# Optimization experiments

Hardware: AMD Instinct MI355X
Metric: run time of the kernel (lower is better)

## Reference

```python
import jax, jax.numpy as jnp
import numpy as np

EMBED = 1024
HEADS = 16
HEAD_DIM = EMBED // HEADS
FF = 4096
EPS = 1e-5


def layer_norm(x, g, b):
    mu = jnp.mean(x, axis=-1, keepdims=True)
    var = jnp.mean(jnp.square(x - mu), axis=-1, keepdims=True)
    return (x - mu) * jax.lax.rsqrt(var + EPS) * g + b


def setup_inputs() -> dict:
    key = jax.random.key(0)
    ks = jax.random.split(key, 16)
    s = 0.02
    x = jax.random.normal(ks[0], (4, 2048, EMBED), dtype=jnp.float32)
    d = {
        "x": x,
        "Wq": jax.random.normal(ks[1], (EMBED, EMBED), jnp.float32) * s,
        "bq": jnp.zeros((EMBED,), jnp.float32),
        "Wk": jax.random.normal(ks[2], (EMBED, EMBED), jnp.float32) * s,
        "bk": jnp.zeros((EMBED,), jnp.float32),
        "Wv": jax.random.normal(ks[3], (EMBED, EMBED), jnp.float32) * s,
        "bv": jnp.zeros((EMBED,), jnp.float32),
        "Wo": jax.random.normal(ks[4], (EMBED, EMBED), jnp.float32) * s,
        "bo": jnp.zeros((EMBED,), jnp.float32),
        "W1": jax.random.normal(ks[5], (EMBED, FF), jnp.float32) * s,
        "b1": jnp.zeros((FF,), jnp.float32),
        "W2": jax.random.normal(ks[6], (FF, EMBED), jnp.float32) * s,
        "b2": jnp.zeros((EMBED,), jnp.float32),
        "ln1_g": jnp.ones((EMBED,), jnp.float32),
        "ln1_b": jnp.zeros((EMBED,), jnp.float32),
        "ln2_g": jnp.ones((EMBED,), jnp.float32),
        "ln2_b": jnp.zeros((EMBED,), jnp.float32),
    }
    return d


def reference(x, Wq, bq, Wk, bk, Wv, bv, Wo, bo, W1, b1, W2, b2, ln1_g, ln1_b, ln2_g, ln2_b):
    B, S, E = x.shape
    scale = np.sqrt(HEAD_DIM).astype(np.float32)
    # project and split heads: (B, H, S, Dh)
    def heads(t):
        return t.reshape(B, S, HEADS, HEAD_DIM).transpose(0, 2, 1, 3)
    Q = heads(x @ Wq + bq)
    K = heads(x @ Wk + bk)
    V = heads(x @ Wv + bv)
    scores = jnp.einsum("bhqd,bhkd->bhqk", Q, K) / scale
    attn = jax.nn.softmax(scores, axis=-1)
    ctx = jnp.einsum("bhqk,bhkd->bhqd", attn, V)
    ctx = ctx.transpose(0, 2, 1, 3).reshape(B, S, E)
    attn_out = ctx @ Wo + bo
    x = layer_norm(x + attn_out, ln1_g, ln1_b)
    ff = jax.nn.relu(x @ W1 + b1) @ W2 + b2
    x = layer_norm(x + ff, ln2_g, ln2_b)
    return x
```

## Files before the change

### kernel.cpp

```cpp
#include <hip/hip_runtime.h>
#include <stdint.h>

typedef uint16_t u16;
typedef __bf16 bf16x8 __attribute__((ext_vector_type(8)));
typedef float f32x4 __attribute__((ext_vector_type(4)));

__device__ __forceinline__ float bf2f(u16 u) {
  union { uint32_t i; float f; } v; v.i = ((uint32_t)u) << 16; return v.f;
}
__device__ __forceinline__ u16 f2bf(float f) {
  union { float f; uint32_t i; } v; v.f = f;
  uint32_t r = v.i + 0x7fffu + ((v.i >> 16) & 1u);
  return (u16)(r >> 16);
}
__device__ __forceinline__ uint32_t pack2(float a, float b) {
  return (uint32_t)f2bf(a) | ((uint32_t)f2bf(b) << 16);
}
__device__ __forceinline__ void gll16(const u16* g, u16* l) {
  __builtin_amdgcn_global_load_lds((const __attribute__((address_space(1))) void*)g,
                                   (__attribute__((address_space(3))) void*)l, 16, 0, 0);
}

__global__ __launch_bounds__(256) void f32_to_bf16(
    const float* __restrict__ in, u16* __restrict__ out)
{
  int idx = blockIdx.x * 256 + threadIdx.x;
  float4 v = *(const float4*)(in + (size_t)idx * 4);
  uint2 o;
  o.x = pack2(v.x, v.y);
  o.y = pack2(v.z, v.w);
  *(uint2*)(out + (size_t)idx * 4) = o;
}

__global__ __launch_bounds__(256) void concat_bias(
    const float* __restrict__ a, const float* __restrict__ b,
    const float* __restrict__ c, float* __restrict__ o, float sa)
{
  int i = blockIdx.x * 256 + threadIdx.x;
  float v = (i < 1024) ? a[i] * sa : ((i < 2048) ? b[i - 1024] : c[i - 2048]);
  o[i] = v;
}

__global__ __launch_bounds__(256) void transpose_f2b(
    const float* __restrict__ in, u16* __restrict__ out, int R, int C, int ldo,
    float scale)
{
  __shared__ u16 tile[32][33];
  int c0 = blockIdx.x * 32, r0 = blockIdx.y * 32;
  int x = threadIdx.x, y = threadIdx.y;
#pragma unroll
  for (int i = 0; i < 32; i += 8)
    tile[y + i][x] = f2bf(in[(size_t)(r0 + y + i) * C + (c0 + x)] * scale);
  __syncthreads();
#pragma unroll
  for (int i = 0; i < 32; i += 8)
    out[(size_t)(c0 + y + i) * ldo + (r0 + x)] = tile[x][y + i];
}

__global__ __launch_bounds__(256) void transpose_v(
    const u16* __restrict__ src, u16* __restrict__ dst)
{
  __shared__ u16 tile[64][72];
  int kc = blockIdx.x;
  int bh = blockIdx.y;
  int b = bh >> 4, h = bh & 15;
  int t = threadIdx.x;
  int r = t >> 3;
  int c0 = (t & 7) * 8;
  const u16* s0 = src + ((size_t)(b * 2048 + kc * 64 + r) * 3072) + h * 64 + c0;
#pragma unroll
  for (int hh = 0; hh < 2; hh++)
    *(uint4*)(&tile[r + hh * 32][c0]) = *(const uint4*)(s0 + (size_t)hh * 32 * 3072);
  __syncthreads();
#pragma unroll
  for (int hh = 0; hh < 2; hh++) {
    int d = r + hh * 32;
    u16 vals[8];
#pragma unroll
    for (int p = 0; p < 8; p++) {
      int pos = c0 + p;
      int key = (pos & 0x23) | ((pos & 4) << 2) | ((pos >> 1) & 0x0C);
      vals[p] = tile[key][d];
    }
    *(uint4*)(dst + ((size_t)bh * 64 + d) * 2048 + (size_t)kc * 64 + c0) = *(uint4*)vals;
  }
}

#define BM 128
#define BN 128
#define BK 64

__global__ __launch_bounds__(256, 3) void gemm_bt(
    const u16* __restrict__ A, const u16* __restrict__ BT,
    const float* __restrict__ bias, u16* __restrict__ C,
    int N, int K, int lda, int ldb, int ldc, int relu, int addC)
{
  __shared__ __align__(16) u16 As[BM][BK];
  __shared__ __align__(16) u16 Bs[BN][BK];
  int tid = threadIdx.x;
  int gx = gridDim.x;
  int id = blockIdx.y * gx + blockIdx.x;
  int cpx = (gx * gridDim.y) >> 3;
  int nid = (id & 7) * cpx + (id >> 3);
  int m0 = (nid / gx) * BM, n0 = (nid % gx) * BN;
  int wave = tid >> 6, lane = tid & 63;
  int quad = lane >> 4, tr = lane & 15;
  int wm = (wave >> 1) * 64, wn = (wave & 1) * 64;
  int tr7 = tr & 7;

  f32x4 zero = {0.f, 0.f, 0.f, 0.f};
  f32x4 acc[4][4];
#pragma unroll
  for (int i = 0; i < 4; i++)
#pragma unroll
    for (int j = 0; j < 4; j++) acc[i][j] = zero;

  int srow = tid >> 3;
  int sblk = (tid & 7) ^ (srow & 7);
  const u16* Abase = A  + (size_t)(m0 + srow) * lda + sblk * 8;
  const u16* Bbase = BT + (size_t)(n0 + srow) * ldb + sblk * 8;
  u16* la = &As[0][0] + tid * 8;
  u16* lb = &Bs[0][0] + tid * 8;

  for (int k0 = 0; k0 < K; k0 += BK) {
#pragma unroll
    for (int R = 0; R < 4; R++) {
      gll16(Abase + (size_t)(R * 32) * lda + k0, la + R * 2048);
      gll16(Bbase + (size_t)(R * 32) * ldb + k0, lb + R * 2048);
    }
    __syncthreads();
#pragma unroll
    for (int ks = 0; ks < 2; ks++) {
      bf16x8 af[4], bfr[4];
#pragma unroll
      for (int i = 0; i < 4; i++)
        af[i]  = *(const bf16x8*)(&As[wm + i*16 + tr][(((ks*4 + quad) ^ tr7)) * 8]);
#pragma unroll
      for (int j = 0; j < 4; j++)
        bfr[j] = *(const bf16x8*)(&Bs[wn + j*16 + tr][(((ks*4 + quad) ^ tr7)) * 8]);
#pragma unroll
      for (int i = 0; i < 4; i++)
#pragma unroll
        for (int j = 0; j < 4; j++)
          acc[i][j] = __builtin_amdgcn_mfma_f32_16x16x32_bf16(af[i], bfr[j], acc[i][j], 0, 0, 0);
    }
    __syncthreads();
  }

#pragma unroll
  for (int j = 0; j < 4; j++) {
    int n = n0 + wn + j*16 + tr;
    float bv = bias ? bias[n] : 0.f;
#pragma unroll
    for (int i = 0; i < 4; i++) {
      int mrow = m0 + wm + i*16 + quad*4;
#pragma unroll
      for (int r = 0; r < 4; r++) {
        size_t idx = (size_t)(mrow + r) * ldc + n;
        float v = acc[i][j][r] + bv;
        if (addC) v += bf2f(C[idx]);
        if (relu) v = v > 0.f ? v : 0.f;
        C[idx] = f2bf(v);
      }
    }
  }
}

__global__ __launch_bounds__(256, 4) void flash_attn(
    const u16* __restrict__ Qb, const u16* __restrict__ Kb,
    const u16* __restrict__ Vtg, u16* __restrict__ Ob, int ldqkv, int ldo)
{
  __shared__ __align__(16) u16 Ks[2][4096];
  __shared__ __align__(16) u16 Vt[2][4096];

  const int S = 2048;
  int tid = threadIdx.x;
  int wv = tid >> 6, lane = tid & 63;
  int quad = lane >> 4, tr = lane & 15, tr7 = tr & 7;
  int id = blockIdx.y * 16 + blockIdx.x;
  int xcd = id & 7, sidx = id >> 3;
  int bh = xcd * 8 + (sidx & 7);
  int q0 = (sidx >> 3) * 128;
  int b = bh >> 4, h = bh & 15;
  int wq = wv * 32;
  size_t rowbase = (size_t)b * S;
  int colbase = h * 64;

  bf16x8 qf[2][2];
#pragma unroll
  for (int i = 0; i < 2; i++)
#pragma unroll
    for (int ks = 0; ks < 2; ks++)
      qf[i][ks] = *(const bf16x8*)(Qb + (rowbase + q0 + wq + i*16 + tr) * ldqkv
                                   + colbase + ks*32 + quad*8);

  f32x4 zero = {0.f, 0.f, 0.f, 0.f};
  f32x4 o[2][4];
  f32x4 lacc[2] = {zero, zero};
#pragma unroll
  for (int i = 0; i < 2; i++)
#pragma unroll
    for (int j = 0; j < 4; j++) o[i][j] = zero;

  bf16x8 onesf;
  {
    union { uint32_t w[4]; bf16x8 v; } u;
    u.w[0] = u.w[1] = u.w[2] = u.w[3] = 0x3F803F80u;
    onesf = u.v;
  }

  int srow = tid >> 3;
  int sblk = (tid & 7) ^ (srow & 7);
  const u16* kg = Kb + (rowbase + srow) * ldqkv + colbase + sblk * 8;
  const u16* vg = Vtg + ((size_t)bh * 64 + srow) * 2048 + sblk * 8;
  size_t kstep32 = (size_t)32 * ldqkv;

  gll16(kg,            &Ks[0][0] + tid * 8);
  gll16(kg + kstep32,  &Ks[0][0] + 2048 + tid * 8);
  gll16(vg,            &Vt[0][0] + tid * 8);
  gll16(vg + 32*2048,  &Vt[0][0] + 2048 + tid * 8);
  __syncthreads();

  for (int kv0 = 0; kv0 < S; kv0 += 64) {
    int cur = (kv0 >> 6) & 1;
    if (kv0 + 64 < S) {
      const u16* kn = kg + (size_t)(kv0 + 64) * ldqkv;
      const u16* vn = vg + (kv0 + 64);
      u16* kd = &Ks[cur ^ 1][0] + tid * 8;
      u16* vd = &Vt[cur ^ 1][0] + tid * 8;
      gll16(kn,           kd);
      gll16(kn + kstep32, kd + 2048);
      gll16(vn,           vd);
      gll16(vn + 32*2048, vd + 2048);
    }

    const u16* kb = &Ks[cur][0];
    const u16* vb = &Vt[cur][0];

    f32x4 s2[4][2];
#pragma unroll
    for (int j = 0; j < 4; j++)
#pragma unroll
      for (int i = 0; i < 2; i++) s2[j][i] = zero;
#pragma unroll
    for (int ks = 0; ks < 2; ks++) {
      bf16x8 kf[4];
#pragma unroll
      for (int j = 0; j < 4; j++)
        kf[j] = *(const bf16x8*)(kb + (size_t)(j*16 + tr) * 64 + ((ks*4 + quad) ^ tr7) * 8);
#pragma unroll
      for (int j = 0; j < 4; j++)
#pragma unroll
        for (int i = 0; i < 2; i++)
          s2[j][i] = __builtin_amdgcn_mfma_f32_16x16x32_bf16(kf[j], qf[i][ks], s2[j][i], 0, 0, 0);
    }

#pragma unroll
    for (int j = 0; j < 4; j++) {
#pragma unroll
      for (int i = 0; i < 2; i++) {
        s2[j][i][0] = __builtin_amdgcn_exp2f(s2[j][i][0]);
        s2[j][i][1] = __builtin_amdgcn_exp2f(s2[j][i][1]);
        s2[j][i][2] = __builtin_amdgcn_exp2f(s2[j][i][2]);
        s2[j][i][3] = __builtin_amdgcn_exp2f(s2[j][i][3]);
      }
    }

#pragma unroll
    for (int ks = 0; ks < 2; ks++) {
      bf16x8 pa[2];
#pragma unroll
      for (int i = 0; i < 2; i++) {
        union { uint32_t w[4]; bf16x8 v; } u;
        u.w[0] = __builtin_amdgcn_perm(__float_as_uint(s2[2*ks][i][1]),
                                       __float_as_uint(s2[2*ks][i][0]), 0x07060302u);
        u.w[1] = __builtin_amdgcn_perm(__float_as_uint(s2[2*ks][i][3]),
                                       __float_as_uint(s2[2*ks][i][2]), 0x07060302u);
        u.w[2] = __builtin_amdgcn_perm(__float_as_uint(s2[2*ks+1][i][1]),
                                       __float_as_uint(s2[2*ks+1][i][0]), 0x07060302u);
        u.w[3] = __builtin_amdgcn_perm(__float_as_uint(s2[2*ks+1][i][3]),
                                       __float_as_uint(s2[2*ks+1][i][2]), 0x07060302u);
        pa[i] = u.v;
      }
#pragma unroll
      for (int i = 0; i < 2; i++)
        lacc[i] = __builtin_amdgcn_mfma_f32_16x16x32_bf16(pa[i], onesf, lacc[i], 0, 0, 0);
#pragma unroll
      for (int jd = 0; jd < 4; jd++) {
        bf16x8 vf = *(const bf16x8*)(vb + (size_t)(jd*16 + tr) * 64 + ((ks*4 + quad) ^ tr7) * 8);
#pragma unroll
        for (int i = 0; i < 2; i++)
          o[i][jd] = __builtin_amdgcn_mfma_f32_16x16x32_bf16(pa[i], vf, o[i][jd], 0, 0, 0);
      }
    }

    __syncthreads();
  }

#pragma unroll
  for (int i = 0; i < 2; i++) {
#pragma unroll
    for (int r = 0; r < 4; r++) {
      float inv = 1.f / lacc[i][r];
      size_t qrow = rowbase + q0 + wq + i*16 + quad*4 + r;
#pragma unroll
      for (int jd = 0; jd < 4; jd++)
        Ob[qrow * ldo + colbase + jd*16 + tr] = f2bf(o[i][jd][r] * inv);
    }
  }
}

__global__ __launch_bounds__(256) void add_ln_a(
    const float* __restrict__ X, const u16* __restrict__ Rr,
    const float* __restrict__ G, const float* __restrict__ Bb,
    u16* __restrict__ Y)
{
  int row = blockIdx.x;
  int tid = threadIdx.x;
  __shared__ float sbuf[4], qbuf[4];
  float4 xv = *(const float4*)(X + (size_t)row * 1024 + tid * 4);
  uint2 ru = *(const uint2*)(Rr + (size_t)row * 1024 + tid * 4);
  const u16* rs = (const u16*)&ru;
  const float* xs = (const float*)&xv;
  float v[4];
  float s = 0.f, q = 0.f;
#pragma unroll
  for (int e = 0; e < 4; e++) {
    float a = xs[e] + bf2f(rs[e]);
    v[e] = a; s += a; q += a * a;
  }
#pragma unroll
  for (int off = 1; off < 64; off <<= 1) {
    s += __shfl_xor(s, off, 64);
    q += __shfl_xor(q, off, 64);
  }
  if ((tid & 63) == 0) { sbuf[tid >> 6] = s; qbuf[tid >> 6] = q; }
  __syncthreads();
  s = sbuf[0] + sbuf[1] + sbuf[2] + sbuf[3];
  q = qbuf[0] + qbuf[1] + qbuf[2] + qbuf[3];
  float mu  = s * (1.f / 1024.f);
  float var = q * (1.f / 1024.f) - mu * mu;
  float inv = rsqrtf(var + 1e-5f);
#pragma unroll
  for (int e = 0; e < 4; e++) {
    int col = tid * 4 + e;
    float yv = (v[e] - mu) * inv * G[col] + Bb[col];
    Y[(size_t)row * 1024 + col] = f2bf(yv);
  }
}

__global__ __launch_bounds__(256) void add_ln_b(
    const u16* __restrict__ X, const u16* __restrict__ Rr,
    const float* __restrict__ G, const float* __restrict__ Bb,
    float* __restrict__ Y)
{
  int row = blockIdx.x;
  int tid = threadIdx.x;
  __shared__ float sbuf[4], qbuf[4];
  uint2 xu = *(const uint2*)(X  + (size_t)row * 1024 + tid * 4);
  uint2 ru = *(const uint2*)(Rr + (size_t)row * 1024 + tid * 4);
  const u16* xs = (const u16*)&xu;
  const u16* rs = (const u16*)&ru;
  float v[4];
  float s = 0.f, q = 0.f;
#pragma unroll
  for (int e = 0; e < 4; e++) {
    float a = bf2f(xs[e]) + bf2f(rs[e]);
    v[e] = a; s += a; q += a * a;
  }
#pragma unroll
  for (int off = 1; off < 64; off <<= 1) {
    s += __shfl_xor(s, off, 64);
    q += __shfl_xor(q, off, 64);
  }
  if ((tid & 63) == 0) { sbuf[tid >> 6] = s; qbuf[tid >> 6] = q; }
  __syncthreads();
  s = sbuf[0] + sbuf[1] + sbuf[2] + sbuf[3];
  q = qbuf[0] + qbuf[1] + qbuf[2] + qbuf[3];
  float mu  = s * (1.f / 1024.f);
  float var = q * (1.f / 1024.f) - mu * mu;
  float inv = rsqrtf(var + 1e-5f);
  float4 yv;
  float* yp = (float*)&yv;
#pragma unroll
  for (int e = 0; e < 4; e++) {
    int col = tid * 4 + e;
    yp[e] = (v[e] - mu) * inv * G[col] + Bb[col];
  }
  *(float4*)(Y + (size_t)row * 1024 + tid * 4) = yv;
}

extern "C" void kernel_launch(void* const* d_in, const int* in_sizes, int n_in,
                              void* d_out, int out_size, void* d_ws, size_t ws_size,
                              hipStream_t stream) {
  const float* x   = (const float*)d_in[0];
  const float* Wq  = (const float*)d_in[1];
  const float* bq  = (const float*)d_in[2];
  const float* Wk  = (const float*)d_in[3];
  const float* bk  = (const float*)d_in[4];
  const float* Wv  = (const float*)d_in[5];
  const float* bv  = (const float*)d_in[6];
  const float* Wo  = (const float*)d_in[7];
  const float* bo  = (const float*)d_in[8];
  const float* W1  = (const float*)d_in[9];
  const float* b1  = (const float*)d_in[10];
  const float* W2  = (const float*)d_in[11];
  const float* b2  = (const float*)d_in[12];
  const float* g1  = (const float*)d_in[13];
  const float* be1 = (const float*)d_in[14];
  const float* g2  = (const float*)d_in[15];
  const float* be2 = (const float*)d_in[16];
  float* out = (float*)d_out;
  u16* ws  = (u16*)d_ws;

  const int Nrow = 8192, E = 1024, FFd = 4096;
  const size_t M1 = 1048576;
  const float SCL = 0.18033688011112042f;
  u16* xb     = ws;
  u16* WqkvT  = ws + 8  * M1;
  u16* WoT    = ws + 11 * M1;
  u16* W1T    = ws + 12 * M1;
  u16* W2T    = ws + 16 * M1;
  u16* QKV    = ws + 20 * M1;
  u16* Vtg    = ws;
  u16* X1     = ws;
  u16* F2     = ws + 20 * M1;
  float* bqkv = (float*)d_out;
  u16*  AO    = (u16*)d_out;
  u16*  Hc    = (u16*)d_out;

  dim3 tb(256);
  dim3 tt(32, 8);
  f32_to_bf16<<<dim3(8192), tb, 0, stream>>>(x, xb);
  transpose_f2b<<<dim3(E/32,  E/32),  tt, 0, stream>>>(Wq, WqkvT,        E,   E,   E,   SCL);
  transpose_f2b<<<dim3(E/32,  E/32),  tt, 0, stream>>>(Wk, WqkvT + 1*M1, E,   E,   E,   1.f);
  transpose_f2b<<<dim3(E/32,  E/32),  tt, 0, stream>>>(Wv, WqkvT + 2*M1, E,   E,   E,   1.f);
  transpose_f2b<<<dim3(E/32,  E/32),  tt, 0, stream>>>(Wo, WoT,          E,   E,   E,   1.f);
  transpose_f2b<<<dim3(FFd/32,E/32),  tt, 0, stream>>>(W1, W1T,          E,   FFd, E,   1.f);
  transpose_f2b<<<dim3(E/32,  FFd/32),tt, 0, stream>>>(W2, W2T,          FFd, E,   FFd, 1.f);
  concat_bias<<<dim3(12), tb, 0, stream>>>(bq, bk, bv, bqkv, SCL);

  gemm_bt<<<dim3(24, Nrow/BM), tb, 0, stream>>>(xb, WqkvT, bqkv, QKV,
                                                3072, E, E, E, 3072, 0, 0);
  transpose_v<<<dim3(32, 64), tb, 0, stream>>>(QKV + 2048, Vtg);
  flash_attn<<<dim3(16, 64), dim3(256), 0, stream>>>(QKV, QKV + 1024, Vtg,
                                                     QKV + 2048, 3072, 3072);
  gemm_bt<<<dim3(8, Nrow/BM), tb, 0, stream>>>(QKV + 2048, WoT, bo, AO,
                                               E, E, 3072, E, E, 0, 0);
  add_ln_a<<<dim3(Nrow), tb, 0, stream>>>(x, AO, g1, be1, X1);

  for (int c = 0; c < 2; c++) {
    gemm_bt<<<dim3(16, Nrow/BM), tb, 0, stream>>>(
        X1, W1T + (size_t)c * 2048 * E, b1 + c * 2048, Hc,
        2048, E, E, E, 2048, 1, 0);
    gemm_bt<<<dim3(8, Nrow/BM), tb, 0, stream>>>(
        Hc, W2T + (size_t)c * 2048, (c == 0 ? b2 : (const float*)nullptr), F2,
        E, 2048, 2048, FFd, E, 0, (c == 0 ? 0 : 1));
  }

  add_ln_b<<<dim3(Nrow), tb, 0, stream>>>(X1, F2, g2, be2, out);
}
```

Baseline: 532.1 us.

## Load K and V fragments directly from global memory in flash attention

Removes the double-buffered LDS staging of K and V tiles (global_load_lds plus a barrier each iteration). Each wave now reads its MFMA fragments straight from global memory, relying on L1/L2 caching, and the loop is unrolled by two. This drops LDS traffic and block-wide synchronisation, but each of the four waves now fetches the same K/V data redundantly and global-load latency is no longer hidden by prefetch.

```diff
diff --git a/kernel.cpp b/kernel.cpp
--- a/kernel.cpp
+++ b/kernel.cpp
@@ -170,13 +170,10 @@
     const u16* __restrict__ Qb, const u16* __restrict__ Kb,
     const u16* __restrict__ Vtg, u16* __restrict__ Ob, int ldqkv, int ldo)
 {
-  __shared__ __align__(16) u16 Ks[2][4096];
-  __shared__ __align__(16) u16 Vt[2][4096];
-
   const int S = 2048;
   int tid = threadIdx.x;
   int wv = tid >> 6, lane = tid & 63;
-  int quad = lane >> 4, tr = lane & 15, tr7 = tr & 7;
+  int quad = lane >> 4, tr = lane & 15;
   int id = blockIdx.y * 16 + blockIdx.x;
   int xcd = id & 7, sidx = id >> 3;
   int bh = xcd * 8 + (sidx & 7);
@@ -209,34 +206,11 @@
     onesf = u.v;
   }
 
-  int srow = tid >> 3;
-  int sblk = (tid & 7) ^ (srow & 7);
-  const u16* kg = Kb + (rowbase + srow) * ldqkv + colbase + sblk * 8;
-  const u16* vg = Vtg + ((size_t)bh * 64 + srow) * 2048 + sblk * 8;
-  size_t kstep32 = (size_t)32 * ldqkv;
-
-  gll16(kg,            &Ks[0][0] + tid * 8);
-  gll16(kg + kstep32,  &Ks[0][0] + 2048 + tid * 8);
-  gll16(vg,            &Vt[0][0] + tid * 8);
-  gll16(vg + 32*2048,  &Vt[0][0] + 2048 + tid * 8);
-  __syncthreads();
-
+  const u16* kp = Kb + (rowbase + tr) * ldqkv + colbase + quad * 8;
+  const u16* vp = Vtg + ((size_t)bh * 64 + tr) * 2048 + quad * 8;
+
+#pragma unroll 2
   for (int kv0 = 0; kv0 < S; kv0 += 64) {
-    int cur = (kv0 >> 6) & 1;
-    if (kv0 + 64 < S) {
-      const u16* kn = kg + (size_t)(kv0 + 64) * ldqkv;
-      const u16* vn = vg + (kv0 + 64);
-      u16* kd = &Ks[cur ^ 1][0] + tid * 8;
-      u16* vd = &Vt[cur ^ 1][0] + tid * 8;
-      gll16(kn,           kd);
-      gll16(kn + kstep32, kd + 2048);
-      gll16(vn,           vd);
-      gll16(vn + 32*2048, vd + 2048);
-    }
-
-    const u16* kb = &Ks[cur][0];
-    const u16* vb = &Vt[cur][0];
-
     f32x4 s2[4][2];
 #pragma unroll
     for (int j = 0; j < 4; j++)
@@ -247,7 +221,7 @@
       bf16x8 kf[4];
 #pragma unroll
       for (int j = 0; j < 4; j++)
-        kf[j] = *(const bf16x8*)(kb + (size_t)(j*16 + tr) * 64 + ((ks*4 + quad) ^ tr7) * 8);
+        kf[j] = *(const bf16x8*)(kp + (size_t)(kv0 + j*16) * ldqkv + ks*32);
 #pragma unroll
       for (int j = 0; j < 4; j++)
 #pragma unroll
@@ -287,14 +261,12 @@
         lacc[i] = __builtin_amdgcn_mfma_f32_16x16x32_bf16(pa[i], onesf, lacc[i], 0, 0, 0);
 #pragma unroll
       for (int jd = 0; jd < 4; jd++) {
-        bf16x8 vf = *(const bf16x8*)(vb + (size_t)(jd*16 + tr) * 64 + ((ks*4 + quad) ^ tr7) * 8);
+        bf16x8 vf = *(const bf16x8*)(vp + (size_t)(jd*16) * 2048 + kv0 + ks*32);
 #pragma unroll
         for (int i = 0; i < 2; i++)
           o[i][jd] = __builtin_amdgcn_mfma_f32_16x16x32_bf16(pa[i], vf, o[i][jd], 0, 0, 0);
       }
     }
-
-    __syncthreads();
   }
 
 #pragma unroll
```

Result: slower. 808.1 us (+51.9%).
